# Optimization experiments

Measured on AMD Instinct MI355X. Metric: run time of the kernel, lower is better.

The kernel has to match this reference:

```python
import jax, jax.numpy as jnp
import numpy as np

T, B, I, H, LBL = 200, 1024, 128, 128, 4


def setup_inputs() -> dict:
    key = jax.random.key(0)
    ks = jax.random.split(key, 14)
    si = 1.0 / np.sqrt(I)
    sh = 1.0 / np.sqrt(H)
    inputs = jax.random.normal(ks[0], (T, B, I), jnp.float32)
    lengths = jnp.maximum(jax.random.randint(ks[1], (B,), 1, T + 1), LBL).astype(jnp.int32)
    return {
        "inputs": inputs,
        "lengths": lengths,
        "Wih_g": jax.random.normal(ks[2], (3 * H, I), jnp.float32) * si,
        "Whh_g": jax.random.normal(ks[3], (3 * H, H), jnp.float32) * sh,
        "bih_g": jax.random.normal(ks[4], (3 * H,), jnp.float32) * sh,
        "bhh_g": jax.random.normal(ks[5], (3 * H,), jnp.float32) * sh,
        "Wih_l": jax.random.normal(ks[6], (3 * H, I), jnp.float32) * si,
        "Whh_l": jax.random.normal(ks[7], (3 * H, H), jnp.float32) * sh,
        "bih_l": jax.random.normal(ks[8], (3 * H,), jnp.float32) * sh,
        "bhh_l": jax.random.normal(ks[9], (3 * H,), jnp.float32) * sh,
        "A1": jax.random.normal(ks[10], (H, H), jnp.float32) * sh,
        "A2": jax.random.normal(ks[11], (H, H), jnp.float32) * sh,
        "v1": jax.random.normal(ks[12], (1, H), jnp.float32) * sh,
        "label_len": LBL,
    }


def gru(x, Wih, Whh, bih, bhh):
    # x: [T, B, I] time-major. PyTorch GRU cell semantics.
    Bq, Hq = x.shape[1], Whh.shape[1]
    gi_all = jnp.einsum('tbi,gi->tbg', x, Wih) + bih  # precompute input projections [T,B,3H]
    def step(h, gi):
        gh = h @ Whh.T + bhh
        ir, iz, inn = jnp.split(gi, 3, axis=-1)
        hr, hz, hn = jnp.split(gh, 3, axis=-1)
        r = jax.nn.sigmoid(ir + hr)
        z = jax.nn.sigmoid(iz + hz)
        n = jnp.tanh(inn + r * hn)
        h = (1.0 - z) * n + z * h
        return h, h
    h0 = jnp.zeros((Bq, Hq), x.dtype)
    _, hs = jax.lax.scan(step, h0, gi_all)
    return hs  # [T, B, H]


def reference(inputs, lengths, Wih_g, Whh_g, bih_g, bhh_g,
              Wih_l, Whh_l, bih_l, bhh_l, A1, A2, v1, label_len):
    h_g = gru(inputs, Wih_g, Whh_g, bih_g, bhh_g)  # [T,B,H]
    h_l = gru(inputs, Wih_l, Whh_l, bih_l, bhh_l)  # [T,B,H]
    # attention score per step s: v1(sigmoid(A1 h_l + A2 h_g)), query-independent
    pre = jax.nn.sigmoid(jnp.einsum('tbh,gh->tbg', h_l, A1) +
                         jnp.einsum('tbh,gh->tbg', h_g, A2))
    scores = jnp.einsum('tbg,og->tbo', pre, v1)  # [T,B,1]
    # per-t output = cumsum_{s<=t}(score*h_l) + h_g[t]
    out = jnp.cumsum(scores * h_l, axis=0) + h_g  # [T,B,H]
    out_b = jnp.transpose(out, (1, 0, 2))  # [B,T,H]
    # gather last label_len timesteps of each sequence: h[b,k] = out[L_b-label_len+k, b]
    idx = lengths[:, None].astype(jnp.int32) - label_len + jnp.arange(label_len, dtype=jnp.int32)[None, :]
    idx = jnp.clip(idx, 0, out_b.shape[1] - 1)  # [B, label_len]
    h = jnp.take_along_axis(out_b, idx[:, :, None], axis=1)  # [B, label_len, H]
    return h
```

## Files before the change

### kernel.cpp

```cpp
#include <hip/hip_runtime.h>
#include <stdint.h>


typedef __attribute__((ext_vector_type(8))) short short8;
typedef __attribute__((ext_vector_type(4))) float float4v;

#define LDS_BARRIER() asm volatile("s_waitcnt lgkmcnt(0)\n\ts_barrier" ::: "memory")

__device__ inline float bf2f(unsigned short u){
  union { unsigned int i; float f; } v; v.i = ((unsigned int)u) << 16; return v.f;
}
__device__ inline unsigned short f2bf(float f){
  union { float f; unsigned int i; } v; v.f = f;
  unsigned int x = v.i;
  return (unsigned short)((x + 0x7fffu + ((x >> 16) & 1u)) >> 16);
}
__device__ inline unsigned int pack2(float a, float b){
  return (unsigned int)f2bf(a) | ((unsigned int)f2bf(b) << 16);
}
__device__ inline float sigm(float x){ return __builtin_amdgcn_rcpf(1.0f + __expf(-x)); }

__global__ void k_prep(unsigned short* hl_slot, unsigned short* hg_slot, float* cum,
                       const float* A1, const float* A2, unsigned short* a12)
{
  int i = blockIdx.x * blockDim.x + threadIdx.x;
  hl_slot[i] = 0;
  hg_slot[i] = 0;
  cum[i] = 0.0f;
  if (i < 32768) {
    a12[i] = f2bf((i < 16384) ? A1[i] : A2[i - 16384]);
  }
}

__global__ __launch_bounds__(512, 2) void k_scan(
    const float* __restrict__ x,
    const float* __restrict__ Wih_g, const float* __restrict__ Whh_g,
    const float* __restrict__ bih_g, const float* __restrict__ bhh_g,
    const float* __restrict__ Wih_l, const float* __restrict__ Whh_l,
    const float* __restrict__ bih_l, const float* __restrict__ bhh_l,
    unsigned short* __restrict__ hl_seq, unsigned short* __restrict__ hg_seq,
    int tc, int t0)
{
  __shared__ __align__(16) unsigned short hbuf[2][16][136];
  __shared__ __align__(16) unsigned short xbuf[2][16][136];
  int tid = threadIdx.x;
  int w = tid >> 6, L = tid & 63, l15 = L & 15, q = L >> 4;
  int gru = blockIdx.x & 1;
  int b0 = (blockIdx.x >> 1) * 16;
  const float* Wih = gru ? Wih_l : Wih_g;
  const float* Whh = gru ? Whh_l : Whh_g;
  const float* bih = gru ? bih_l : bih_g;
  const float* bhh = gru ? bhh_l : bhh_g;
  unsigned short* myseq = gru ? hl_seq : hg_seq;

  int col = w * 16 + l15;

  short8 Wi[3][4], Wh[3][4];
  #pragma unroll
  for (int G = 0; G < 3; G++) {
    int row = G * 128 + col;
    #pragma unroll
    for (int kf = 0; kf < 4; kf++) {
      const float4* p0 = (const float4*)(Wih + (size_t)row * 128 + kf * 32 + q * 8);
      const float4* p1 = (const float4*)(Whh + (size_t)row * 128 + kf * 32 + q * 8);
      float4 a0 = p0[0], a1 = p0[1], b0f = p1[0], b1f = p1[1];
      short8 si, sh;
      si[0]=(short)f2bf(a0.x); si[1]=(short)f2bf(a0.y); si[2]=(short)f2bf(a0.z); si[3]=(short)f2bf(a0.w);
      si[4]=(short)f2bf(a1.x); si[5]=(short)f2bf(a1.y); si[6]=(short)f2bf(a1.z); si[7]=(short)f2bf(a1.w);
      sh[0]=(short)f2bf(b0f.x); sh[1]=(short)f2bf(b0f.y); sh[2]=(short)f2bf(b0f.z); sh[3]=(short)f2bf(b0f.w);
      sh[4]=(short)f2bf(b1f.x); sh[5]=(short)f2bf(b1f.y); sh[6]=(short)f2bf(b1f.z); sh[7]=(short)f2bf(b1f.w);
      Wi[G][kf] = si; Wh[G][kf] = sh;
    }
  }
  float br  = bih[col]       + bhh[col];
  float bz  = bih[128 + col] + bhh[128 + col];
  float bin = bih[256 + col];
  float bnh = bhh[256 + col];

  float hold[4];
  #pragma unroll
  for (int r = 0; r < 4; r++) {
    int m = q * 4 + r;
    unsigned short u = myseq[((size_t)(tc - 1) * 1024 + b0 + m) * 128 + col];
    hold[r] = bf2f(u);
    hbuf[0][m][col] = u;
  }
  int xrow = tid >> 5, xc4 = (tid & 31) * 4;
  {
    float4 x0 = ((const float4*)(x + ((size_t)t0 * 1024 + b0) * 128))[tid];
    *(uint2*)&xbuf[0][xrow][xc4] = make_uint2(pack2(x0.x, x0.y), pack2(x0.z, x0.w));
  }
  int tn = t0 + (tc > 1 ? 1 : 0);
  float4 xr = ((const float4*)(x + ((size_t)tn * 1024 + b0) * 128))[tid];
  __syncthreads();

  unsigned short* opq = myseq + ((size_t)(b0 + q * 4)) * 128 + col;

  auto step = [&](int s, int pin, int pout) {
    short8 Ax[4], Ah[4];
    #pragma unroll
    for (int kf = 0; kf < 4; kf++) Ax[kf] = *(const short8*)&xbuf[pin][l15][kf * 32 + q * 8];
    #pragma unroll
    for (int kf = 0; kf < 4; kf++) Ah[kf] = *(const short8*)&hbuf[pin][l15][kf * 32 + q * 8];

    *(uint2*)&xbuf[pout][xrow][xc4] = make_uint2(pack2(xr.x, xr.y), pack2(xr.z, xr.w));
    {
      int t2 = t0 + (s + 2 < tc ? s + 2 : tc - 1);
      xr = ((const float4*)(x + ((size_t)t2 * 1024 + b0) * 128))[tid];
    }

    float4v rx = (float4v){0.f,0.f,0.f,0.f}, zx = rx, nx = rx;
    float4v rh = rx, zh = rx, nh = rx;
    #pragma unroll
    for (int kf = 0; kf < 4; kf++) rx = __builtin_amdgcn_mfma_f32_16x16x32_bf16(Ax[kf], Wi[0][kf], rx, 0,0,0);
    #pragma unroll
    for (int kf = 0; kf < 4; kf++) zx = __builtin_amdgcn_mfma_f32_16x16x32_bf16(Ax[kf], Wi[1][kf], zx, 0,0,0);
    #pragma unroll
    for (int kf = 0; kf < 4; kf++) nx = __builtin_amdgcn_mfma_f32_16x16x32_bf16(Ax[kf], Wi[2][kf], nx, 0,0,0);
    #pragma unroll
    for (int kf = 0; kf < 4; kf++) rh = __builtin_amdgcn_mfma_f32_16x16x32_bf16(Ah[kf], Wh[0][kf], rh, 0,0,0);
    #pragma unroll
    for (int kf = 0; kf < 4; kf++) zh = __builtin_amdgcn_mfma_f32_16x16x32_bf16(Ah[kf], Wh[1][kf], zh, 0,0,0);
    #pragma unroll
    for (int kf = 0; kf < 4; kf++) nh = __builtin_amdgcn_mfma_f32_16x16x32_bf16(Ah[kf], Wh[2][kf], nh, 0,0,0);

    float cr[4], cz[4], cn[4];
    #pragma unroll
    for (int r = 0; r < 4; r++) { cr[r] = rx[r] + br; cz[r] = zx[r] + bz; cn[r] = nx[r] + bin; }

    #pragma unroll
    for (int r = 0; r < 4; r++) {
      float er = __expf(-(rh[r] + cr[r]));
      float ez = __expf(-(zh[r] + cz[r]));
      float pr = 1.0f + er, pz = 1.0f + ez;
      float inv = __builtin_amdgcn_rcpf(pr * pz);
      float rr = pz * inv;
      float zz = pr * inv;
      float y  = cn[r] + rr * (nh[r] + bnh);
      float em = __expf(-2.0f * y);
      float nn = 2.0f * __builtin_amdgcn_rcpf(1.0f + em) - 1.0f;
      float hn = nn + zz * (hold[r] - nn);
      hold[r] = hn;
      unsigned short hu = f2bf(hn);
      hbuf[pout][q * 4 + r][col] = hu;
      opq[r * 128] = hu;
    }
    opq += 131072;
    LDS_BARRIER();
  };

  int s = 0;
  for (; s + 1 < tc; s += 2) { step(s, 0, 1); step(s + 1, 1, 0); }
  if (s < tc) step(s, 0, 1);
}

__global__ __launch_bounds__(512) void k_score(const unsigned short* __restrict__ hl_seq,
                                               const unsigned short* __restrict__ hg_seq,
                                               const unsigned short* __restrict__ a12,
                                               const float* __restrict__ v1,
                                               float* __restrict__ score, int tc)
{
  __shared__ __align__(16) unsigned short M1[128][136];
  __shared__ __align__(16) unsigned short M2[128][136];
  int tid = threadIdx.x;
  int w = tid >> 6, L = tid & 63;
  int l15 = L & 15, q = L >> 4;
  int s = blockIdx.x;
  int bhalf = blockIdx.y * 512;

  #pragma unroll
  for (int it = 0; it < 4; it++) {
    int f8 = it * 512 + tid;
    *(short8*)&M1[f8 >> 4][(f8 & 15) * 8] = *(const short8*)(a12 + (size_t)f8 * 8);
    *(short8*)&M2[f8 >> 4][(f8 & 15) * 8] = *(const short8*)(a12 + 16384 + (size_t)f8 * 8);
  }
  __syncthreads();

  float v1v[8];
  #pragma unroll
  for (int nt = 0; nt < 8; nt++) v1v[nt] = v1[nt * 16 + l15];

  short8 Fl[4], Fg[4], Pl[4], Pg[4];
  {
    size_t base = ((size_t)s * 1024 + bhalf + (size_t)w * 16 + l15) * 128;
    #pragma unroll
    for (int kf = 0; kf < 4; kf++) {
      Fl[kf] = *(const short8*)(hl_seq + base + kf * 32 + q * 8);
      Fg[kf] = *(const short8*)(hg_seq + base + kf * 32 + q * 8);
    }
  }
  #pragma unroll
  for (int it = 0; it < 4; it++) {
    int b0 = bhalf + (it * 8 + w) * 16;
    if (it + 1 < 4) {
      size_t base = ((size_t)s * 1024 + bhalf + (size_t)((it + 1) * 8 + w) * 16 + l15) * 128;
      #pragma unroll
      for (int kf = 0; kf < 4; kf++) {
        Pl[kf] = *(const short8*)(hl_seq + base + kf * 32 + q * 8);
        Pg[kf] = *(const short8*)(hg_seq + base + kf * 32 + q * 8);
      }
    }
    float4v acc[8];
    #pragma unroll
    for (int nt = 0; nt < 8; nt++) {
      float4v a = (float4v){0.f, 0.f, 0.f, 0.f};
      #pragma unroll
      for (int kf = 0; kf < 4; kf++)
        a = __builtin_amdgcn_mfma_f32_16x16x32_bf16(
            Fl[kf], *(const short8*)&M1[nt * 16 + l15][kf * 32 + q * 8], a, 0, 0, 0);
      #pragma unroll
      for (int kf = 0; kf < 4; kf++)
        a = __builtin_amdgcn_mfma_f32_16x16x32_bf16(
            Fg[kf], *(const short8*)&M2[nt * 16 + l15][kf * 32 + q * 8], a, 0, 0, 0);
      acc[nt] = a;
    }
    float p4[4];
    #pragma unroll
    for (int r = 0; r < 4; r++) {
      float sum = 0.f;
      #pragma unroll
      for (int nt = 0; nt < 8; nt++) sum += v1v[nt] * sigm(acc[nt][r]);
      sum += __shfl_xor(sum, 1, 16);
      sum += __shfl_xor(sum, 2, 16);
      sum += __shfl_xor(sum, 4, 16);
      sum += __shfl_xor(sum, 8, 16);
      p4[r] = sum;
    }
    if (l15 == 0) {
      #pragma unroll
      for (int r = 0; r < 4; r++)
        score[(size_t)(b0 + q * 4 + r) * tc + s] = p4[r];
    }
    #pragma unroll
    for (int kf = 0; kf < 4; kf++) { Fl[kf] = Pl[kf]; Fg[kf] = Pg[kf]; }
  }
}

__global__ __launch_bounds__(256) void k_cum(const float* __restrict__ score,
                                             const unsigned short* __restrict__ hl_seq,
                                             const unsigned short* __restrict__ hg_seq,
                                             const int* __restrict__ lengths,
                                             float* __restrict__ cum,
                                             float* __restrict__ out, int tc, int t0)
{
  __shared__ __align__(16) unsigned short hlL[100 * 256];
  __shared__ float scL[2][100];
  int tid = threadIdx.x;
  int b2 = tid >> 7, j = tid & 127;
  int b0 = blockIdx.x * 2;
  int b = b0 + b2;
  int base = b2 * 128 + j;

  float c = cum[(size_t)b * 128 + j];
  int cap0 = lengths[b] - 4;

  float hgv[4];
  #pragma unroll
  for (int d = 0; d < 4; d++) {
    int sl = cap0 + d - t0;
    hgv[d] = (sl >= 0 && sl < tc) ? bf2f(hg_seq[((size_t)sl * 1024 + b) * 128 + j]) : 0.f;
  }

  for (int seg = 0; seg < tc; seg += 100) {
    int len = (tc - seg < 100) ? (tc - seg) : 100;
    __syncthreads();
    for (int f8 = tid; f8 < len * 32; f8 += 256) {
      int sl = f8 >> 5, r8 = f8 & 31;
      *(short8*)&hlL[(size_t)f8 * 8] =
          *(const short8*)(hl_seq + ((size_t)(seg + sl) * 1024 + b0) * 128 + r8 * 8);
    }
    for (int i = tid; i < 2 * len; i += 256) {
      int bb = (i >= len) ? 1 : 0;
      int sl = i - bb * len;
      scL[bb][sl] = score[(size_t)(b0 + bb) * tc + seg + sl];
    }
    __syncthreads();

    int sl = 0;
    for (; sl + 5 <= len; sl += 5) {
      float h[5], sc[5];
      #pragma unroll
      for (int k = 0; k < 5; k++) {
        h[k] = bf2f(hlL[(size_t)(sl + k) * 256 + base]);
        sc[k] = scL[b2][sl + k];
      }
      #pragma unroll
      for (int k = 0; k < 5; k++) {
        c += sc[k] * h[k];
        int d = (t0 + seg + sl + k) - cap0;
        if ((unsigned)d < 4u)
          out[((size_t)b * 4 + d) * 128 + j] = c + hgv[d];
      }
    }
    for (; sl < len; sl++) {
      c += scL[b2][sl] * bf2f(hlL[(size_t)sl * 256 + base]);
      int d = (t0 + seg + sl) - cap0;
      if ((unsigned)d < 4u)
        out[((size_t)b * 4 + d) * 128 + j] = c + hgv[d];
    }
  }
  cum[(size_t)b * 128 + j] = c;
}

extern "C" void kernel_launch(void* const* d_in, const int* in_sizes, int n_in,
                              void* d_out, int out_size, void* d_ws, size_t ws_size,
                              hipStream_t stream)
{
  const float* x     = (const float*)d_in[0];
  const int* lengths = (const int*)d_in[1];
  const float* Wih_g = (const float*)d_in[2];
  const float* Whh_g = (const float*)d_in[3];
  const float* bih_g = (const float*)d_in[4];
  const float* bhh_g = (const float*)d_in[5];
  const float* Wih_l = (const float*)d_in[6];
  const float* Whh_l = (const float*)d_in[7];
  const float* bih_l = (const float*)d_in[8];
  const float* bhh_l = (const float*)d_in[9];
  const float* A1    = (const float*)d_in[10];
  const float* A2    = (const float*)d_in[11];
  const float* v1    = (const float*)d_in[12];
  float* out = (float*)d_out;

  const size_t fixed = 65536 + 524288;
  const int cands[7] = {200, 100, 50, 10, 4, 2, 1};
  int tc = 0;
  for (int i = 0; i < 7; i++) {
    int T = cands[i];
    size_t need = 2 * (size_t)T * 1024 * 128 * 2
                + (size_t)T * 1024 * 4
                + fixed;
    if (need <= ws_size) { tc = T; break; }
  }
  if (!tc) return;

  char* wsb = (char*)d_ws;
  size_t o = 0;
  unsigned short* a12 = (unsigned short*)(wsb + o); o += 65536;
  float* cum   = (float*)(wsb + o); o += 524288;
  unsigned short* hl  = (unsigned short*)(wsb + o); o += (size_t)tc * 1024 * 128 * 2;
  unsigned short* hg  = (unsigned short*)(wsb + o); o += (size_t)tc * 1024 * 128 * 2;
  float* score = (float*)(wsb + o);

  unsigned short* hl_slot = hl + (size_t)(tc - 1) * 1024 * 128;
  unsigned short* hg_slot = hg + (size_t)(tc - 1) * 1024 * 128;

  k_prep<<<512, 256, 0, stream>>>(hl_slot, hg_slot, cum, A1, A2, a12);
  int nch = 200 / tc;
  for (int c = 0; c < nch; c++) {
    k_scan<<<128, 512, 0, stream>>>(x, Wih_g, Whh_g, bih_g, bhh_g,
                                    Wih_l, Whh_l, bih_l, bhh_l, hl, hg, tc, c * tc);
    k_score<<<dim3(tc, 2), 512, 0, stream>>>(hl, hg, a12, v1, score, tc);
    k_cum<<<512, 256, 0, stream>>>(score, hl, hg, lengths, cum, out, tc, c * tc);
  }
}
```

Baseline: 401.5 us.

## Precompute GRU input projections in separate blocks overlapped with recurrent scan

Result: slower. 502.3 us (+25.1%).

```diff
diff --git a/kernel.cpp b/kernel.cpp
--- a/kernel.cpp
+++ b/kernel.cpp
@@ -9,6 +9,9 @@
 
 __device__ inline float bf2f(unsigned short u){
   union { unsigned int i; float f; } v; v.i = ((unsigned int)u) << 16; return v.f;
+}
+__device__ inline float u2f(unsigned int b){
+  union { unsigned int i; float f; } v; v.i = b; return v.f;
 }
 __device__ inline unsigned short f2bf(float f){
   union { float f; unsigned int i; } v; v.f = f;
@@ -32,49 +35,142 @@
   }
 }
 
+__device__ __forceinline__ void gi_gemm(
+    const float* __restrict__ x,
+    const float* __restrict__ Wih, const float* __restrict__ bih,
+    const float* __restrict__ bhh,
+    unsigned short* __restrict__ gi, int gtc, int t0g, int bid2, int tid,
+    unsigned short (*xbuf)[16][136])
+{
+  int w = tid >> 6, L = tid & 63, l15 = L & 15, q = L >> 4;
+  int b0 = (bid2 >> 1) * 16;
+  int col = w * 16 + l15;
+
+  short8 Wi[3][4];
+  #pragma unroll
+  for (int G = 0; G < 3; G++) {
+    int row = G * 128 + col;
+    #pragma unroll
+    for (int kf = 0; kf < 4; kf++) {
+      const float4* p0 = (const float4*)(Wih + (size_t)row * 128 + kf * 32 + q * 8);
+      float4 a0 = p0[0], a1 = p0[1];
+      short8 si;
+      si[0]=(short)f2bf(a0.x); si[1]=(short)f2bf(a0.y); si[2]=(short)f2bf(a0.z); si[3]=(short)f2bf(a0.w);
+      si[4]=(short)f2bf(a1.x); si[5]=(short)f2bf(a1.y); si[6]=(short)f2bf(a1.z); si[7]=(short)f2bf(a1.w);
+      Wi[G][kf] = si;
+    }
+  }
+  float bias0 = bih[col]       + bhh[col];
+  float bias1 = bih[128 + col] + bhh[128 + col];
+  float bias2 = bih[256 + col];
+
+  int xrow = tid >> 5, xc4 = (tid & 31) * 4;
+  {
+    float4 x0 = ((const float4*)(x + ((size_t)t0g * 1024 + b0) * 128))[tid];
+    *(uint2*)&xbuf[0][xrow][xc4] = make_uint2(pack2(x0.x, x0.y), pack2(x0.z, x0.w));
+  }
+  int tn = t0g + (gtc > 1 ? 1 : 0);
+  float4 xr = ((const float4*)(x + ((size_t)tn * 1024 + b0) * 128))[tid];
+  __syncthreads();
+
+  int cur = 0;
+  for (int s = 0; s < gtc; s++) {
+    short8 Ax[4];
+    #pragma unroll
+    for (int kf = 0; kf < 4; kf++) Ax[kf] = *(const short8*)&xbuf[cur][l15][kf * 32 + q * 8];
+
+    if (s + 1 < gtc) {
+      *(uint2*)&xbuf[cur ^ 1][xrow][xc4] = make_uint2(pack2(xr.x, xr.y), pack2(xr.z, xr.w));
+      int t2 = t0g + (s + 2 < gtc ? s + 2 : gtc - 1);
+      xr = ((const float4*)(x + ((size_t)t2 * 1024 + b0) * 128))[tid];
+    }
+
+    float4v ar = (float4v){0.f,0.f,0.f,0.f}, az = ar, an = ar;
+    #pragma unroll
+    for (int kf = 0; kf < 4; kf++) ar = __builtin_amdgcn_mfma_f32_16x16x32_bf16(Ax[kf], Wi[0][kf], ar, 0,0,0);
+    #pragma unroll
+    for (int kf = 0; kf < 4; kf++) az = __builtin_amdgcn_mfma_f32_16x16x32_bf16(Ax[kf], Wi[1][kf], az, 0,0,0);
+    #pragma unroll
+    for (int kf = 0; kf < 4; kf++) an = __builtin_amdgcn_mfma_f32_16x16x32_bf16(Ax[kf], Wi[2][kf], an, 0,0,0);
+
+    uint2* outp = (uint2*)(gi + ((size_t)s * 128 + bid2) * 6144) + tid;
+    outp[0]    = make_uint2(pack2(ar[0] + bias0, ar[1] + bias0), pack2(ar[2] + bias0, ar[3] + bias0));
+    outp[512]  = make_uint2(pack2(az[0] + bias1, az[1] + bias1), pack2(az[2] + bias1, az[3] + bias1));
+    outp[1024] = make_uint2(pack2(an[0] + bias2, an[1] + bias2), pack2(an[2] + bias2, an[3] + bias2));
+
+    LDS_BARRIER();
+    cur ^= 1;
+  }
+}
+
+__global__ __launch_bounds__(512, 2) void k_gi(
+    const float* __restrict__ x,
+    const float* __restrict__ Wih_g, const float* __restrict__ bih_g, const float* __restrict__ bhh_g,
+    const float* __restrict__ Wih_l, const float* __restrict__ bih_l, const float* __restrict__ bhh_l,
+    unsigned short* __restrict__ gi, int tcg)
+{
+  __shared__ __align__(16) unsigned short xbuf[2][16][136];
+  __shared__ unsigned long long ldspad[9400];
+  int tid = threadIdx.x;
+  if (tcg == 0) ldspad[tid] = 0;
+  int bid = blockIdx.x;
+  const float* Wih = (bid & 1) ? Wih_l : Wih_g;
+  const float* bih = (bid & 1) ? bih_l : bih_g;
+  const float* bhh = (bid & 1) ? bhh_l : bhh_g;
+  gi_gemm(x, Wih, bih, bhh, gi, tcg, 0, bid, tid, xbuf);
+}
+
 __global__ __launch_bounds__(512, 2) void k_scan(
     const float* __restrict__ x,
-    const float* __restrict__ Wih_g, const float* __restrict__ Whh_g,
-    const float* __restrict__ bih_g, const float* __restrict__ bhh_g,
-    const float* __restrict__ Wih_l, const float* __restrict__ Whh_l,
-    const float* __restrict__ bih_l, const float* __restrict__ bhh_l,
+    const float* __restrict__ Whh_g, const float* __restrict__ bhh_g,
+    const float* __restrict__ Whh_l, const float* __restrict__ bhh_l,
+    const float* __restrict__ Wih_g, const float* __restrict__ bih_g,
+    const float* __restrict__ Wih_l, const float* __restrict__ bih_l,
     unsigned short* __restrict__ hl_seq, unsigned short* __restrict__ hg_seq,
-    int tc, int t0)
+    const unsigned short* __restrict__ gi_rd, unsigned short* __restrict__ gi_wr,
+    int tc, int t0, int gtc, int t0g)
 {
   __shared__ __align__(16) unsigned short hbuf[2][16][136];
   __shared__ __align__(16) unsigned short xbuf[2][16][136];
+  __shared__ unsigned long long ldspad[9400];
   int tid = threadIdx.x;
+  if (tc == 0) ldspad[tid] = 0;
+  int bid = blockIdx.x;
+
+  if (bid >= 128) {
+    if (gtc > 0) {
+      int bid2 = bid - 128;
+      const float* Wih = (bid2 & 1) ? Wih_l : Wih_g;
+      const float* bih = (bid2 & 1) ? bih_l : bih_g;
+      const float* bhh = (bid2 & 1) ? bhh_l : bhh_g;
+      gi_gemm(x, Wih, bih, bhh, gi_wr, gtc, t0g, bid2, tid, xbuf);
+    }
+    return;
+  }
+
   int w = tid >> 6, L = tid & 63, l15 = L & 15, q = L >> 4;
-  int gru = blockIdx.x & 1;
-  int b0 = (blockIdx.x >> 1) * 16;
-  const float* Wih = gru ? Wih_l : Wih_g;
+  int gru = bid & 1;
+  int b0 = (bid >> 1) * 16;
   const float* Whh = gru ? Whh_l : Whh_g;
-  const float* bih = gru ? bih_l : bih_g;
   const float* bhh = gru ? bhh_l : bhh_g;
   unsigned short* myseq = gru ? hl_seq : hg_seq;
 
   int col = w * 16 + l15;
 
-  short8 Wi[3][4], Wh[3][4];
+  short8 Wh[3][4];
   #pragma unroll
   for (int G = 0; G < 3; G++) {
     int row = G * 128 + col;
     #pragma unroll
     for (int kf = 0; kf < 4; kf++) {
-      const float4* p0 = (const float4*)(Wih + (size_t)row * 128 + kf * 32 + q * 8);
       const float4* p1 = (const float4*)(Whh + (size_t)row * 128 + kf * 32 + q * 8);
-      float4 a0 = p0[0], a1 = p0[1], b0f = p1[0], b1f = p1[1];
-      short8 si, sh;
-      si[0]=(short)f2bf(a0.x); si[1]=(short)f2bf(a0.y); si[2]=(short)f2bf(a0.z); si[3]=(short)f2bf(a0.w);
-      si[4]=(short)f2bf(a1.x); si[5]=(short)f2bf(a1.y); si[6]=(short)f2bf(a1.z); si[7]=(short)f2bf(a1.w);
+      float4 b0f = p1[0], b1f = p1[1];
+      short8 sh;
       sh[0]=(short)f2bf(b0f.x); sh[1]=(short)f2bf(b0f.y); sh[2]=(short)f2bf(b0f.z); sh[3]=(short)f2bf(b0f.w);
       sh[4]=(short)f2bf(b1f.x); sh[5]=(short)f2bf(b1f.y); sh[6]=(short)f2bf(b1f.z); sh[7]=(short)f2bf(b1f.w);
-      Wi[G][kf] = si; Wh[G][kf] = sh;
-    }
-  }
-  float br  = bih[col]       + bhh[col];
-  float bz  = bih[128 + col] + bhh[128 + col];
-  float bin = bih[256 + col];
+      Wh[G][kf] = sh;
+    }
+  }
   float bnh = bhh[256 + col];
 
   float hold[4];
@@ -85,38 +181,23 @@
     hold[r] = bf2f(u);
     hbuf[0][m][col] = u;
   }
-  int xrow = tid >> 5, xc4 = (tid & 31) * 4;
-  {
-    float4 x0 = ((const float4*)(x + ((size_t)t0 * 1024 + b0) * 128))[tid];
-    *(uint2*)&xbuf[0][xrow][xc4] = make_uint2(pack2(x0.x, x0.y), pack2(x0.z, x0.w));
-  }
-  int tn = t0 + (tc > 1 ? 1 : 0);
-  float4 xr = ((const float4*)(x + ((size_t)tn * 1024 + b0) * 128))[tid];
+
+  const uint2* gbase = (const uint2*)gi_rd + (size_t)bid * 1536 + tid;
+  uint2 gc0 = gbase[0], gc1 = gbase[512], gc2 = gbase[1024];
+  const uint2* gptr = gbase + 196608;
   __syncthreads();
 
   unsigned short* opq = myseq + ((size_t)(b0 + q * 4)) * 128 + col;
 
-  auto step = [&](int s, int pin, int pout) {
-    short8 Ax[4], Ah[4];
-    #pragma unroll
-    for (int kf = 0; kf < 4; kf++) Ax[kf] = *(const short8*)&xbuf[pin][l15][kf * 32 + q * 8];
+  auto step = [&](int pin, int pout) {
+    short8 Ah[4];
     #pragma unroll
     for (int kf = 0; kf < 4; kf++) Ah[kf] = *(const short8*)&hbuf[pin][l15][kf * 32 + q * 8];
 
-    *(uint2*)&xbuf[pout][xrow][xc4] = make_uint2(pack2(xr.x, xr.y), pack2(xr.z, xr.w));
-    {
-      int t2 = t0 + (s + 2 < tc ? s + 2 : tc - 1);
-      xr = ((const float4*)(x + ((size_t)t2 * 1024 + b0) * 128))[tid];
-    }
-
-    float4v rx = (float4v){0.f,0.f,0.f,0.f}, zx = rx, nx = rx;
-    float4v rh = rx, zh = rx, nh = rx;
-    #pragma unroll
-    for (int kf = 0; kf < 4; kf++) rx = __builtin_amdgcn_mfma_f32_16x16x32_bf16(Ax[kf], Wi[0][kf], rx, 0,0,0);
-    #pragma unroll
-    for (int kf = 0; kf < 4; kf++) zx = __builtin_amdgcn_mfma_f32_16x16x32_bf16(Ax[kf], Wi[1][kf], zx, 0,0,0);
-    #pragma unroll
-    for (int kf = 0; kf < 4; kf++) nx = __builtin_amdgcn_mfma_f32_16x16x32_bf16(Ax[kf], Wi[2][kf], nx, 0,0,0);
+    uint2 gn0 = gptr[0], gn1 = gptr[512], gn2 = gptr[1024];
+    gptr += 196608;
+
+    float4v rh = (float4v){0.f,0.f,0.f,0.f}, zh = rh, nh = rh;
     #pragma unroll
     for (int kf = 0; kf < 4; kf++) rh = __builtin_amdgcn_mfma_f32_16x16x32_bf16(Ah[kf], Wh[0][kf], rh, 0,0,0);
     #pragma unroll
@@ -125,8 +206,12 @@
     for (int kf = 0; kf < 4; kf++) nh = __builtin_amdgcn_mfma_f32_16x16x32_bf16(Ah[kf], Wh[2][kf], nh, 0,0,0);
 
     float cr[4], cz[4], cn[4];
-    #pragma unroll
-    for (int r = 0; r < 4; r++) { cr[r] = rx[r] + br; cz[r] = zx[r] + bz; cn[r] = nx[r] + bin; }
+    cr[0]=u2f(gc0.x<<16); cr[1]=u2f(gc0.x & 0xffff0000u);
+    cr[2]=u2f(gc0.y<<16); cr[3]=u2f(gc0.y & 0xffff0000u);
+    cz[0]=u2f(gc1.x<<16); cz[1]=u2f(gc1.x & 0xffff0000u);
+    cz[2]=u2f(gc1.y<<16); cz[3]=u2f(gc1.y & 0xffff0000u);
+    cn[0]=u2f(gc2.x<<16); cn[1]=u2f(gc2.x & 0xffff0000u);
+    cn[2]=u2f(gc2.y<<16); cn[3]=u2f(gc2.y & 0xffff0000u);
 
     #pragma unroll
     for (int r = 0; r < 4; r++) {
@@ -145,16 +230,17 @@
       hbuf[pout][q * 4 + r][col] = hu;
       opq[r * 128] = hu;
     }
+    gc0 = gn0; gc1 = gn1; gc2 = gn2;
     opq += 131072;
     LDS_BARRIER();
   };
 
   int s = 0;
-  for (; s + 1 < tc; s += 2) { step(s, 0, 1); step(s + 1, 1, 0); }
-  if (s < tc) step(s, 0, 1);
-}
-
-__global__ __launch_bounds__(512) void k_score(const unsigned short* __restrict__ hl_seq,
+  for (; s + 1 < tc; s += 2) { step(0, 1); step(1, 0); }
+  if (s < tc) step(0, 1);
+}
+
+__global__ __launch_bounds__(256) void k_score(const unsigned short* __restrict__ hl_seq,
                                                const unsigned short* __restrict__ hg_seq,
                                                const unsigned short* __restrict__ a12,
                                                const float* __restrict__ v1,
@@ -166,11 +252,11 @@
   int w = tid >> 6, L = tid & 63;
   int l15 = L & 15, q = L >> 4;
   int s = blockIdx.x;
-  int bhalf = blockIdx.y * 512;
-
-  #pragma unroll
-  for (int it = 0; it < 4; it++) {
-    int f8 = it * 512 + tid;
+  int bq = blockIdx.y * 256;
+
+  #pragma unroll
+  for (int it = 0; it < 8; it++) {
+    int f8 = it * 256 + tid;
     *(short8*)&M1[f8 >> 4][(f8 & 15) * 8] = *(const short8*)(a12 + (size_t)f8 * 8);
     *(short8*)&M2[f8 >> 4][(f8 & 15) * 8] = *(const short8*)(a12 + 16384 + (size_t)f8 * 8);
   }
@@ -182,7 +268,7 @@
 
   short8 Fl[4], Fg[4], Pl[4], Pg[4];
   {
-    size_t base = ((size_t)s * 1024 + bhalf + (size_t)w * 16 + l15) * 128;
+    size_t base = ((size_t)s * 1024 + bq + (size_t)w * 16 + l15) * 128;
     #pragma unroll
     for (int kf = 0; kf < 4; kf++) {
       Fl[kf] = *(const short8*)(hl_seq + base + kf * 32 + q * 8);
@@ -191,9 +277,9 @@
   }
   #pragma unroll
   for (int it = 0; it < 4; it++) {
-    int b0 = bhalf + (it * 8 + w) * 16;
+    int b0 = bq + (it * 4 + w) * 16;
     if (it + 1 < 4) {
-      size_t base = ((size_t)s * 1024 + bhalf + (size_t)((it + 1) * 8 + w) * 16 + l15) * 128;
+      size_t base = ((size_t)s * 1024 + bq + (size_t)((it + 1) * 4 + w) * 16 + l15) * 128;
       #pragma unroll
       for (int kf = 0; kf < 4; kf++) {
         Pl[kf] = *(const short8*)(hl_seq + base + kf * 32 + q * 8);
@@ -322,13 +408,14 @@
   float* out = (float*)d_out;
 
   const size_t fixed = 65536 + 524288;
-  const int cands[7] = {200, 100, 50, 10, 4, 2, 1};
+  const int cands[6] = {50, 25, 10, 5, 2, 1};
   int tc = 0;
-  for (int i = 0; i < 7; i++) {
+  for (int i = 0; i < 6; i++) {
     int T = cands[i];
-    size_t need = 2 * (size_t)T * 1024 * 128 * 2
-                + (size_t)T * 1024 * 4
-                + fixed;
+    size_t need = fixed
+                + 2 * (size_t)T * 1572864
+                + 2 * (size_t)T * 262144
+                + (size_t)T * 4096;
     if (need <= ws_size) { tc = T; break; }
   }
   if (!tc) return;
@@ -337,19 +424,27 @@
   size_t o = 0;
   unsigned short* a12 = (unsigned short*)(wsb + o); o += 65536;
   float* cum   = (float*)(wsb + o); o += 524288;
-  unsigned short* hl  = (unsigned short*)(wsb + o); o += (size_t)tc * 1024 * 128 * 2;
-  unsigned short* hg  = (unsigned short*)(wsb + o); o += (size_t)tc * 1024 * 128 * 2;
+  unsigned short* gi0 = (unsigned short*)(wsb + o); o += (size_t)tc * 1572864;
+  unsigned short* gi1 = (unsigned short*)(wsb + o); o += (size_t)tc * 1572864;
+  unsigned short* hl  = (unsigned short*)(wsb + o); o += (size_t)tc * 262144;
+  unsigned short* hg  = (unsigned short*)(wsb + o); o += (size_t)tc * 262144;
   float* score = (float*)(wsb + o);
 
-  unsigned short* hl_slot = hl + (size_t)(tc - 1) * 1024 * 128;
-  unsigned short* hg_slot = hg + (size_t)(tc - 1) * 1024 * 128;
+  unsigned short* hl_slot = hl + (size_t)(tc - 1) * 131072;
+  unsigned short* hg_slot = hg + (size_t)(tc - 1) * 131072;
 
   k_prep<<<512, 256, 0, stream>>>(hl_slot, hg_slot, cum, A1, A2, a12);
+  k_gi<<<128, 512, 0, stream>>>(x, Wih_g, bih_g, bhh_g, Wih_l, bih_l, bhh_l, gi0, tc);
+
   int nch = 200 / tc;
   for (int c = 0; c < nch; c++) {
-    k_scan<<<128, 512, 0, stream>>>(x, Wih_g, Whh_g, bih_g, bhh_g,
-                                    Wih_l, Whh_l, bih_l, bhh_l, hl, hg, tc, c * tc);
-    k_score<<<dim3(tc, 2), 512, 0, stream>>>(hl, hg, a12, v1, score, tc);
+    unsigned short* rd = (c & 1) ? gi1 : gi0;
+    unsigned short* wr = (c & 1) ? gi0 : gi1;
+    int gtc = (c + 1 < nch) ? tc : 0;
+    k_scan<<<256, 512, 0, stream>>>(x, Whh_g, bhh_g, Whh_l, bhh_l,
+                                    Wih_g, bih_g, Wih_l, bih_l,
+                                    hl, hg, rd, wr, tc, c * tc, gtc, (c + 1) * tc);
+    k_score<<<dim3(tc, 4), 256, 0, stream>>>(hl, hg, a12, v1, score, tc);
     k_cum<<<512, 256, 0, stream>>>(score, hl, hg, lengths, cum, out, tc, c * tc);
   }
 }
```

## Software-pipeline input projection one step ahead and use packed bf16 conversion

Applied to the files above, without the earlier changes.

Result: no change. 399.7 us (-0.4%).

```diff
diff --git a/kernel.cpp b/kernel.cpp
--- a/kernel.cpp
+++ b/kernel.cpp
@@ -15,8 +15,10 @@
   unsigned int x = v.i;
   return (unsigned short)((x + 0x7fffu + ((x >> 16) & 1u)) >> 16);
 }
-__device__ inline unsigned int pack2(float a, float b){
-  return (unsigned int)f2bf(a) | ((unsigned int)f2bf(b) << 16);
+__device__ inline unsigned int cvt_pk_bf16(float a, float b){
+  unsigned int r;
+  asm("v_cvt_pk_bf16_f32 %0, %1, %2" : "=v"(r) : "v"(a), "v"(b));
+  return r;
 }
 __device__ inline float sigm(float x){ return __builtin_amdgcn_rcpf(1.0f + __expf(-x)); }
 
@@ -88,46 +90,67 @@
   int xrow = tid >> 5, xc4 = (tid & 31) * 4;
   {
     float4 x0 = ((const float4*)(x + ((size_t)t0 * 1024 + b0) * 128))[tid];
-    *(uint2*)&xbuf[0][xrow][xc4] = make_uint2(pack2(x0.x, x0.y), pack2(x0.z, x0.w));
+    *(uint2*)&xbuf[0][xrow][xc4] = make_uint2(cvt_pk_bf16(x0.x, x0.y), cvt_pk_bf16(x0.z, x0.w));
   }
   int tn = t0 + (tc > 1 ? 1 : 0);
   float4 xr = ((const float4*)(x + ((size_t)tn * 1024 + b0) * 128))[tid];
   __syncthreads();
 
+  float4v cx0 = (float4v){0.f,0.f,0.f,0.f}, cx1 = cx0, cx2 = cx0;
+  {
+    short8 Ax[4];
+    #pragma unroll
+    for (int kf = 0; kf < 4; kf++) Ax[kf] = *(const short8*)&xbuf[0][l15][kf * 32 + q * 8];
+    #pragma unroll
+    for (int kf = 0; kf < 4; kf++) cx0 = __builtin_amdgcn_mfma_f32_16x16x32_bf16(Ax[kf], Wi[0][kf], cx0, 0,0,0);
+    #pragma unroll
+    for (int kf = 0; kf < 4; kf++) cx1 = __builtin_amdgcn_mfma_f32_16x16x32_bf16(Ax[kf], Wi[1][kf], cx1, 0,0,0);
+    #pragma unroll
+    for (int kf = 0; kf < 4; kf++) cx2 = __builtin_amdgcn_mfma_f32_16x16x32_bf16(Ax[kf], Wi[2][kf], cx2, 0,0,0);
+  }
+  *(uint2*)&xbuf[1][xrow][xc4] = make_uint2(cvt_pk_bf16(xr.x, xr.y), cvt_pk_bf16(xr.z, xr.w));
+  {
+    int t2 = t0 + (2 < tc ? 2 : tc - 1);
+    xr = ((const float4*)(x + ((size_t)t2 * 1024 + b0) * 128))[tid];
+  }
+  LDS_BARRIER();
+
   unsigned short* opq = myseq + ((size_t)(b0 + q * 4)) * 128 + col;
 
   auto step = [&](int s, int pin, int pout) {
-    short8 Ax[4], Ah[4];
-    #pragma unroll
-    for (int kf = 0; kf < 4; kf++) Ax[kf] = *(const short8*)&xbuf[pin][l15][kf * 32 + q * 8];
-    #pragma unroll
-    for (int kf = 0; kf < 4; kf++) Ah[kf] = *(const short8*)&hbuf[pin][l15][kf * 32 + q * 8];
-
-    *(uint2*)&xbuf[pout][xrow][xc4] = make_uint2(pack2(xr.x, xr.y), pack2(xr.z, xr.w));
+    short8 Ah[4], Axn[4];
+    #pragma unroll
+    for (int kf = 0; kf < 4; kf++) Ah[kf]  = *(const short8*)&hbuf[pin][l15][kf * 32 + q * 8];
+    #pragma unroll
+    for (int kf = 0; kf < 4; kf++) Axn[kf] = *(const short8*)&xbuf[pout][l15][kf * 32 + q * 8];
+
+    float4v rh = (float4v){0.f,0.f,0.f,0.f}, zh = rh, nh = rh;
+    #pragma unroll
+    for (int kf = 0; kf < 4; kf++) rh = __builtin_amdgcn_mfma_f32_16x16x32_bf16(Ah[kf], Wh[0][kf], rh, 0,0,0);
+    #pragma unroll
+    for (int kf = 0; kf < 4; kf++) zh = __builtin_amdgcn_mfma_f32_16x16x32_bf16(Ah[kf], Wh[1][kf], zh, 0,0,0);
+    #pragma unroll
+    for (int kf = 0; kf < 4; kf++) nh = __builtin_amdgcn_mfma_f32_16x16x32_bf16(Ah[kf], Wh[2][kf], nh, 0,0,0);
+
+    float4v nx0 = (float4v){0.f,0.f,0.f,0.f}, nx1 = nx0, nx2 = nx0;
+    #pragma unroll
+    for (int kf = 0; kf < 4; kf++) nx0 = __builtin_amdgcn_mfma_f32_16x16x32_bf16(Axn[kf], Wi[0][kf], nx0, 0,0,0);
+    #pragma unroll
+    for (int kf = 0; kf < 4; kf++) nx1 = __builtin_amdgcn_mfma_f32_16x16x32_bf16(Axn[kf], Wi[1][kf], nx1, 0,0,0);
+    #pragma unroll
+    for (int kf = 0; kf < 4; kf++) nx2 = __builtin_amdgcn_mfma_f32_16x16x32_bf16(Axn[kf], Wi[2][kf], nx2, 0,0,0);
+
+    *(uint2*)&xbuf[pin][xrow][xc4] = make_uint2(cvt_pk_bf16(xr.x, xr.y), cvt_pk_bf16(xr.z, xr.w));
     {
-      int t2 = t0 + (s + 2 < tc ? s + 2 : tc - 1);
-      xr = ((const float4*)(x + ((size_t)t2 * 1024 + b0) * 128))[tid];
-    }
-
-    float4v rx = (float4v){0.f,0.f,0.f,0.f}, zx = rx, nx = rx;
-    float4v rh = rx, zh = rx, nh = rx;
-    #pragma unroll
-    for (int kf = 0; kf < 4; kf++) rx = __builtin_amdgcn_mfma_f32_16x16x32_bf16(Ax[kf], Wi[0][kf], rx, 0,0,0);
-    #pragma unroll
-    for (int kf = 0; kf < 4; kf++) zx = __builtin_amdgcn_mfma_f32_16x16x32_bf16(Ax[kf], Wi[1][kf], zx, 0,0,0);
-    #pragma unroll
-    for (int kf = 0; kf < 4; kf++) nx = __builtin_amdgcn_mfma_f32_16x16x32_bf16(Ax[kf], Wi[2][kf], nx, 0,0,0);
-    #pragma unroll
-    for (int kf = 0; kf < 4; kf++) rh = __builtin_amdgcn_mfma_f32_16x16x32_bf16(Ah[kf], Wh[0][kf], rh, 0,0,0);
-    #pragma unroll
-    for (int kf = 0; kf < 4; kf++) zh = __builtin_amdgcn_mfma_f32_16x16x32_bf16(Ah[kf], Wh[1][kf], zh, 0,0,0);
-    #pragma unroll
-    for (int kf = 0; kf < 4; kf++) nh = __builtin_amdgcn_mfma_f32_16x16x32_bf16(Ah[kf], Wh[2][kf], nh, 0,0,0);
+      int t3 = t0 + (s + 3 < tc ? s + 3 : tc - 1);
+      xr = ((const float4*)(x + ((size_t)t3 * 1024 + b0) * 128))[tid];
+    }
 
     float cr[4], cz[4], cn[4];
     #pragma unroll
-    for (int r = 0; r < 4; r++) { cr[r] = rx[r] + br; cz[r] = zx[r] + bz; cn[r] = nx[r] + bin; }
-
+    for (int r = 0; r < 4; r++) { cr[r] = cx0[r] + br; cz[r] = cx1[r] + bz; cn[r] = cx2[r] + bin; }
+
+    float hnv[4];
     #pragma unroll
     for (int r = 0; r < 4; r++) {
       float er = __expf(-(rh[r] + cr[r]));
@@ -139,12 +162,23 @@
       float y  = cn[r] + rr * (nh[r] + bnh);
       float em = __expf(-2.0f * y);
       float nn = 2.0f * __builtin_amdgcn_rcpf(1.0f + em) - 1.0f;
-      float hn = nn + zz * (hold[r] - nn);
-      hold[r] = hn;
-      unsigned short hu = f2bf(hn);
-      hbuf[pout][q * 4 + r][col] = hu;
-      opq[r * 128] = hu;
-    }
+      hnv[r] = nn + zz * (hold[r] - nn);
+      hold[r] = hnv[r];
+    }
+    unsigned int p01 = cvt_pk_bf16(hnv[0], hnv[1]);
+    unsigned int p23 = cvt_pk_bf16(hnv[2], hnv[3]);
+    unsigned short h0 = (unsigned short)p01, h1 = (unsigned short)(p01 >> 16);
+    unsigned short h2 = (unsigned short)p23, h3 = (unsigned short)(p23 >> 16);
+    hbuf[pout][q * 4 + 0][col] = h0;
+    hbuf[pout][q * 4 + 1][col] = h1;
+    hbuf[pout][q * 4 + 2][col] = h2;
+    hbuf[pout][q * 4 + 3][col] = h3;
+    opq[0]       = h0;
+    opq[128]     = h1;
+    opq[256]     = h2;
+    opq[384]     = h3;
+
+    cx0 = nx0; cx1 = nx1; cx2 = nx2;
     opq += 131072;
     LDS_BARRIER();
   };
```
